# Optimization experiments

Measured on AMD Instinct MI355X. Metric: run time of the kernel, lower is better.

Reference implementation:

```python
import jax, jax.numpy as jnp
import numpy as np

N_BASIS = 8
BASIS_MAX_R = 2.0
BASIS_SIGMA = 0.25


def _radial_basis(difference_mat):
    # difference_mat: [n, b, a, 3] -> gaussian radial basis [n, b, a, K]
    r = jnp.linalg.norm(difference_mat, axis=-1)  # [n, b, a]
    centers = jnp.linspace(0.0, BASIS_MAX_R, N_BASIS, dtype=difference_mat.dtype)
    return jnp.exp(-((r[..., None] - centers) ** 2) / (2.0 * BASIS_SIGMA ** 2))


def setup_inputs() -> dict:
    key = jax.random.key(0)
    k1, k2, k3, k4 = jax.random.split(key, 4)
    n, c, d, p = 2, 8, 8, 1024
    input = jax.random.normal(k1, (n, c, p), dtype=jnp.float32)
    difference_mat = jax.random.normal(k2, (n, p, p, 3), dtype=jnp.float32)
    relative_mask = jax.random.uniform(k3, (n, p, p), dtype=jnp.float32)
    W = jax.random.normal(k4, (d, c, N_BASIS), dtype=jnp.float32) * 0.1
    return {"input": input, "difference_mat": difference_mat,
            "relative_mask": relative_mask, "W": W}


def reference(input, difference_mat, relative_mask, W):
    # kernel(difference_mat): [d, c, n, b, a] pairwise channel-mixing tensor
    basis = _radial_basis(difference_mat)                      # [n, b, a, K]
    kernel = jnp.einsum('dck,nbak->dcnba', W, basis)           # [d, c, n, b, a]
    # masked einsum: 'nba,dcnba->dcnba'
    kernel = kernel * relative_mask[None, None]                # broadcast mask
    # contraction: 'nca,dcnba->ndb'
    output = jnp.einsum('nca,dcnba->ndb', input, kernel)       # [n, d, b]
    return output
```

## Files before the change

### kernel.cpp

```cpp
#include <hip/hip_runtime.h>

#define P 1024
#define C 8
#define D 8
#define K 8
#define WPB 4
#define NITER (P / 64)
#define CHUNK 4
#define NCHUNK (NITER / CHUNK)

__global__ __launch_bounds__(256, 2) void se3_conv_kernel(
    const float* __restrict__ input,
    const float* __restrict__ diff,
    const float* __restrict__ mask,
    const float* __restrict__ W,
    float* __restrict__ out)
{
    __shared__ float inp_lds[C * P];
    __shared__ float Tl[WPB][64];

    const int n    = blockIdx.y;
    const int tid  = threadIdx.x;
    const int lane = tid & 63;
    const int wave = tid >> 6;
    const int b    = blockIdx.x * WPB + wave;

    const float* diff_row = diff + (((size_t)n * P + b) * P) * 3;
    const float* mask_row = mask + ((size_t)n * P + b) * P;

    float xv[NITER], yv[NITER], zv[NITER], mv[NITER];

    #pragma unroll
    for (int j = 0; j < CHUNK; ++j) {
        const float* p = diff_row + (size_t)(lane + j * 64) * 3;
        xv[j] = p[0];
        yv[j] = p[1];
        zv[j] = p[2];
        mv[j] = mask_row[lane + j * 64];
    }

    {
        const float4* src = (const float4*)(input + (size_t)n * C * P);
        float4* dst = (float4*)inp_lds;
        #pragma unroll
        for (int i = 0; i < (C * P / 4) / 256; ++i)
            dst[tid + i * 256] = src[tid + i * 256];
    }

    float acc[K * C];
    #pragma unroll
    for (int i = 0; i < K * C; ++i) acc[i] = 0.0f;

    __syncthreads();

    const float L2E = 1.44269504f;

    #pragma unroll
    for (int ch = 0; ch < NCHUNK; ++ch) {
        if (ch + 1 < NCHUNK) {
            #pragma unroll
            for (int jj = 0; jj < CHUNK; ++jj) {
                const int j = (ch + 1) * CHUNK + jj;
                const float* p = diff_row + (size_t)(lane + j * 64) * 3;
                xv[j] = p[0];
                yv[j] = p[1];
                zv[j] = p[2];
                mv[j] = mask_row[lane + j * 64];
            }
        }

        #pragma unroll
        for (int jj = 0; jj < CHUNK; ++jj) {
            const int j = ch * CHUNK + jj;
            const int a = lane + j * 64;
            const float x = xv[j], y = yv[j], z = zv[j], m = mv[j];

            const float r2 = fmaf(x, x, fmaf(y, y, z * z));
            const float r  = __builtin_amdgcn_sqrtf(r2);
            const float u  = -8.0f * L2E * r2;

            float basis[K];
            #pragma unroll
            for (int k = 0; k < K; ++k) {
                const float ck = (2.0f / 7.0f) * (float)k;
                const float c1 = 16.0f * L2E * ck;
                const float c0 = -8.0f * L2E * ck * ck;
                basis[k] = __builtin_amdgcn_exp2f(fmaf(c1, r, u + c0)) * m;
            }

            float inp[C];
            #pragma unroll
            for (int c = 0; c < C; ++c) inp[c] = inp_lds[c * P + a];

            #pragma unroll
            for (int k = 0; k < K; ++k)
                #pragma unroll
                for (int c = 0; c < C; ++c)
                    acc[k * C + c] = fmaf(basis[k], inp[c], acc[k * C + c]);
        }
    }

    #pragma unroll
    for (int s = 0; s < 6; ++s) {
        const int half = 32 >> s;
        const int bit  = (lane >> s) & 1;
        #pragma unroll
        for (int i = 0; i < half; ++i) {
            const float send = bit ? acc[i] : acc[i + half];
            const float recv = __shfl_xor(send, 1 << s, 64);
            const float keep = bit ? acc[i + half] : acc[i];
            acc[i] = keep + recv;
        }
    }

    const int j64 = (int)(__brev((unsigned)lane) >> 26);
    Tl[wave][j64] = acc[0];
    __syncthreads();

    const int d  = lane >> 3;
    const int k8 = lane & 7;
    float part = 0.0f;
    #pragma unroll
    for (int q = 0; q < 8; ++q)
        part += W[d * 64 + q * 8 + k8] * Tl[wave][k8 * 8 + q];
    part += __shfl_xor(part, 1, 64);
    part += __shfl_xor(part, 2, 64);
    part += __shfl_xor(part, 4, 64);
    if (k8 == 0)
        out[((size_t)n * D + d) * P + b] = part;
}

extern "C" void kernel_launch(void* const* d_in, const int* in_sizes, int n_in,
                              void* d_out, int out_size, void* d_ws, size_t ws_size,
                              hipStream_t stream) {
    const float* input = (const float*)d_in[0];
    const float* diff  = (const float*)d_in[1];
    const float* mask  = (const float*)d_in[2];
    const float* W     = (const float*)d_in[3];
    float* out = (float*)d_out;

    dim3 grid(P / WPB, 2);
    se3_conv_kernel<<<grid, 256, 0, stream>>>(input, diff, mask, W, out);
}
```

Baseline: 14.87 us.

## Split rows across wave pairs, drop LDS staging, use recurrence for Gaussian basis

Each row of pairwise data is now split between two waves, so the grid has twice as many blocks and each wave carries half the register state, allowing four blocks per CU. The input tile is read directly from global memory (L2/L1 cached) instead of being staged in LDS with a barrier. The eight Gaussian basis values come from two exp2 calls and a multiplicative recurrence instead of eight exp2 calls, with a 2^64 scaling to avoid underflow. This risks small precision drift from the recurrence, plus extra global loads for the input in place of LDS reads.

```diff
diff --git a/kernel.cpp b/kernel.cpp
--- a/kernel.cpp
+++ b/kernel.cpp
@@ -4,56 +4,49 @@
 #define C 8
 #define D 8
 #define K 8
-#define WPB 4
-#define NITER (P / 64)
-#define CHUNK 4
+#define NITER 8
+#define CHUNK 2
 #define NCHUNK (NITER / CHUNK)
 
-__global__ __launch_bounds__(256, 2) void se3_conv_kernel(
+__global__ __launch_bounds__(256, 4) void se3_conv_kernel(
     const float* __restrict__ input,
     const float* __restrict__ diff,
     const float* __restrict__ mask,
     const float* __restrict__ W,
     float* __restrict__ out)
 {
-    __shared__ float inp_lds[C * P];
-    __shared__ float Tl[WPB][64];
+    __shared__ float red[4][64];
 
     const int n    = blockIdx.y;
     const int tid  = threadIdx.x;
     const int lane = tid & 63;
     const int wave = tid >> 6;
-    const int b    = blockIdx.x * WPB + wave;
+    const int rsel = wave >> 1;
+    const int half = wave & 1;
+    const int b    = blockIdx.x * 2 + rsel;
 
-    const float* diff_row = diff + (((size_t)n * P + b) * P) * 3;
-    const float* mask_row = mask + ((size_t)n * P + b) * P;
+    const float* diff_row = diff + (((size_t)n * P + b) * P + half * (P / 2)) * 3;
+    const float* mask_row = mask + ((size_t)n * P + b) * P + half * (P / 2);
+    const float* inp_n    = input + (size_t)n * C * P;
+
+    float acc[K * C];
+    #pragma unroll
+    for (int i = 0; i < K * C; ++i) acc[i] = 0.0f;
 
     float xv[NITER], yv[NITER], zv[NITER], mv[NITER];
 
     #pragma unroll
     for (int j = 0; j < CHUNK; ++j) {
         const float* p = diff_row + (size_t)(lane + j * 64) * 3;
-        xv[j] = p[0];
-        yv[j] = p[1];
-        zv[j] = p[2];
+        xv[j] = p[0]; yv[j] = p[1]; zv[j] = p[2];
         mv[j] = mask_row[lane + j * 64];
     }
 
-    {
-        const float4* src = (const float4*)(input + (size_t)n * C * P);
-        float4* dst = (float4*)inp_lds;
-        #pragma unroll
-        for (int i = 0; i < (C * P / 4) / 256; ++i)
-            dst[tid + i * 256] = src[tid + i * 256];
-    }
-
-    float acc[K * C];
-    #pragma unroll
-    for (int i = 0; i < K * C; ++i) acc[i] = 0.0f;
-
-    __syncthreads();
-
-    const float L2E = 1.44269504f;
+    const float C_R2 = -11.5415603f;
+    const float C_R  = 6.5951774f;
+    const float cq[K - 1] = {
+        0.5204502f, 0.1409736f, 0.0381853f, 0.0103432f,
+        0.00280164f, 0.00075888f, 0.00020556f};
 
     #pragma unroll
     for (int ch = 0; ch < NCHUNK; ++ch) {
@@ -62,9 +55,7 @@
             for (int jj = 0; jj < CHUNK; ++jj) {
                 const int j = (ch + 1) * CHUNK + jj;
                 const float* p = diff_row + (size_t)(lane + j * 64) * 3;
-                xv[j] = p[0];
-                yv[j] = p[1];
-                zv[j] = p[2];
+                xv[j] = p[0]; yv[j] = p[1]; zv[j] = p[2];
                 mv[j] = mask_row[lane + j * 64];
             }
         }
@@ -72,62 +63,61 @@
         #pragma unroll
         for (int jj = 0; jj < CHUNK; ++jj) {
             const int j = ch * CHUNK + jj;
-            const int a = lane + j * 64;
-            const float x = xv[j], y = yv[j], z = zv[j], m = mv[j];
-
-            const float r2 = fmaf(x, x, fmaf(y, y, z * z));
-            const float r  = __builtin_amdgcn_sqrtf(r2);
-            const float u  = -8.0f * L2E * r2;
-
-            float basis[K];
-            #pragma unroll
-            for (int k = 0; k < K; ++k) {
-                const float ck = (2.0f / 7.0f) * (float)k;
-                const float c1 = 16.0f * L2E * ck;
-                const float c0 = -8.0f * L2E * ck * ck;
-                basis[k] = __builtin_amdgcn_exp2f(fmaf(c1, r, u + c0)) * m;
-            }
+            const int a = half * (P / 2) + j * 64 + lane;
 
             float inp[C];
             #pragma unroll
-            for (int c = 0; c < C; ++c) inp[c] = inp_lds[c * P + a];
+            for (int c = 0; c < C; ++c) inp[c] = inp_n[c * P + a];
+
+            const float x = xv[j], y = yv[j], z = zv[j];
+            const float r2 = fmaf(x, x, fmaf(y, y, z * z));
+            const float r  = __builtin_amdgcn_sqrtf(r2);
+            float t        = __builtin_amdgcn_exp2f(fmaf(C_R2, r2, 64.0f));
+            const float B  = __builtin_amdgcn_exp2f(C_R * r);
+            const float mp = mv[j] * 0x1p-64f;
 
             #pragma unroll
-            for (int k = 0; k < K; ++k)
+            for (int k = 0; k < K; ++k) {
+                const float bm = t * mp;
                 #pragma unroll
                 for (int c = 0; c < C; ++c)
-                    acc[k * C + c] = fmaf(basis[k], inp[c], acc[k * C + c]);
+                    acc[k * C + c] = fmaf(bm, inp[c], acc[k * C + c]);
+                if (k < K - 1) t = t * (B * cq[k]);
+            }
         }
     }
 
     #pragma unroll
     for (int s = 0; s < 6; ++s) {
-        const int half = 32 >> s;
-        const int bit  = (lane >> s) & 1;
+        const int hw  = 32 >> s;
+        const int bit = (lane >> s) & 1;
         #pragma unroll
-        for (int i = 0; i < half; ++i) {
-            const float send = bit ? acc[i] : acc[i + half];
+        for (int i = 0; i < hw; ++i) {
+            const float send = bit ? acc[i] : acc[i + hw];
             const float recv = __shfl_xor(send, 1 << s, 64);
-            const float keep = bit ? acc[i + half] : acc[i];
+            const float keep = bit ? acc[i + hw] : acc[i];
             acc[i] = keep + recv;
         }
     }
 
     const int j64 = (int)(__brev((unsigned)lane) >> 26);
-    Tl[wave][j64] = acc[0];
+    red[wave][j64] = acc[0];
     __syncthreads();
 
-    const int d  = lane >> 3;
-    const int k8 = lane & 7;
-    float part = 0.0f;
-    #pragma unroll
-    for (int q = 0; q < 8; ++q)
-        part += W[d * 64 + q * 8 + k8] * Tl[wave][k8 * 8 + q];
-    part += __shfl_xor(part, 1, 64);
-    part += __shfl_xor(part, 2, 64);
-    part += __shfl_xor(part, 4, 64);
-    if (k8 == 0)
-        out[((size_t)n * D + d) * P + b] = part;
+    if (half == 0) {
+        const int d  = lane >> 3;
+        const int k8 = lane & 7;
+        float part = 0.0f;
+        #pragma unroll
+        for (int c = 0; c < C; ++c)
+            part += W[d * 64 + c * 8 + k8] *
+                    (red[wave][k8 * 8 + c] + red[wave + 1][k8 * 8 + c]);
+        part += __shfl_xor(part, 1, 64);
+        part += __shfl_xor(part, 2, 64);
+        part += __shfl_xor(part, 4, 64);
+        if (k8 == 0)
+            out[((size_t)n * D + d) * P + b] = part;
+    }
 }
 
 extern "C" void kernel_launch(void* const* d_in, const int* in_sizes, int n_in,
@@ -139,6 +129,6 @@
     const float* W     = (const float*)d_in[3];
     float* out = (float*)d_out;
 
-    dim3 grid(P / WPB, 2);
+    dim3 grid(P / 2, 2);
     se3_conv_kernel<<<grid, 256, 0, stream>>>(input, diff, mask, W, out);
 }
```

Result: slower. 15.60 us (+4.9%).
